# Optimization experiments

Hardware: AMD Instinct MI355X
Metric: run time of the kernel (lower is better)

## Reference

```python
import jax, jax.numpy as jnp
import numpy as np


def setup_inputs() -> dict:
    key = jax.random.key(0)
    k1, k2, k3, k4 = jax.random.split(key, 4)
    B, Q, K, H, D = 2, 2048, 2048, 16, 64
    qs = jax.random.normal(k1, (B, Q, H, D), dtype=jnp.float32)
    ks = jax.random.normal(k2, (B, K, H, D), dtype=jnp.float32)
    vs = jax.random.normal(k3, (B, K, H, D), dtype=jnp.float32)
    # valid lengths in [1, K] so no row is fully masked
    valid_lens = jnp.maximum(jax.random.randint(k4, (B,), 0, K + 1, dtype=jnp.int32), 1)
    return {"qs": qs, "ks": ks, "vs": vs, "valid_lens": valid_lens}


def reference(qs, ks, vs, valid_lens):
    # Faithful math of ScanAttention: scaled dot-product attention with a
    # per-batch key-validity mask (online-softmax scan == exact softmax).
    B, Q, H, D = qs.shape
    K = ks.shape[1]
    scale = 1.0 / jnp.sqrt(jnp.float32(D))
    # [B, H, Q, K]
    scores = jnp.einsum('bqhd,bkhd->bhqk', qs * scale, ks)
    ks_mask = jnp.arange(K)[None, :] < valid_lens[:, None]  # [B, K]
    scores = jnp.where(ks_mask[:, None, None, :], scores, -jnp.inf)
    attn = jax.nn.softmax(scores, axis=-1)
    out = jnp.einsum('bhqk,bkhd->bqhd', attn, vs)  # [B, Q, H, D]
    return out
```

## Files before the change

kernel.cpp:

```cpp
#include <hip/hip_runtime.h>
#include <hip/hip_bf16.h>

typedef __bf16 bf16t;
typedef bf16t bf16x4 __attribute__((ext_vector_type(4)));
typedef bf16t bf16x8 __attribute__((ext_vector_type(8)));
typedef float f32x2 __attribute__((ext_vector_type(2)));
typedef float f32x4 __attribute__((ext_vector_type(4)));
typedef float f32x16 __attribute__((ext_vector_type(16)));
typedef unsigned short u16x8 __attribute__((ext_vector_type(8)));
typedef unsigned int u32x4 __attribute__((ext_vector_type(4)));

#define NB 2
#define NQ 2048
#define NK 2048
#define NH 16
#define ND 64
#define HD (NH * ND)
#define KVBLK 64
#define NUNITS 512
#define SCALE_LOG2E 0.18033688011112042f
#define RESCALE_THR 8.0f

#define OPART_BYTES(n) ((size_t)(n) * 8388608ULL)
#define ML_BYTES(n)    ((size_t)(n) * 524288ULL)

__device__ inline unsigned cvt_pk_bf16(float a, float b) {
    unsigned r;
    asm("v_cvt_pk_bf16_f32 %0, %1, %2" : "=v"(r) : "v"(a), "v"(b));
    return r;
}

__device__ inline void plswap(unsigned& a, unsigned& b) {
#if __has_builtin(__builtin_amdgcn_permlane32_swap)
    auto r = __builtin_amdgcn_permlane32_swap(a, b, false, false);
    a = r[0]; b = r[1];
#else
    const unsigned as = __shfl_xor((int)a, 32);
    const unsigned bs = __shfl_xor((int)b, 32);
    const bool lh = (threadIdx.x & 32) != 0;
    const unsigned na = lh ? bs : a;
    const unsigned nb = lh ? b : as;
    a = na; b = nb;
#endif
}

template <int NSPLIT>
__global__ __launch_bounds__(256, 3)
void scan_attn(const float* __restrict__ qs, const float* __restrict__ ks,
               const float* __restrict__ vs, const int* __restrict__ vlen,
               float* __restrict__ out, char* __restrict__ ws)
{
    const int bid = blockIdx.x;
    const int x    = bid & 7;
    const int jj   = bid >> 3;
    const int b    = jj & 1;
    const int code = x | ((jj >> 1) << 3);
    const int qt   = code / (16 * NSPLIT);
    const int rr   = code % (16 * NSPLIT);
    const int h    = rr / NSPLIT;
    const int s    = rr % NSPLIT;
    const int uidx = ((b * NH + h) << 4) + qt;

    const int tid  = threadIdx.x;
    const int wq   = tid >> 6;
    const int lane = tid & 63;
    const int ql   = lane & 31;
    const int lh   = lane >> 5;
    const int swq  = (ql & 7) << 4;
    const int q    = qt * 128 + wq * 32 + ql;

    const int nkv    = vlen[b];
    const int ntiles = (nkv + KVBLK - 1) >> 6;
    const int rem    = nkv & 63;
    const int tlo    = (ntiles * s) / NSPLIT;
    const int thi    = (ntiles * (s + 1)) / NSPLIT;

    const float* qptr = qs + ((size_t)b * NQ + q) * HD + h * ND;
    const float* kptr = ks + (size_t)b * NK * HD + h * ND;
    const float* vptr = vs + (size_t)b * NK * HD + h * ND;

    __shared__ __align__(16) char smem[2][16384];

    bf16x8 qf[4];
#pragma unroll
    for (int c = 0; c < 4; ++c) {
        const float* p = qptr + 16 * c + 8 * lh;
        f32x4 lo4 = *reinterpret_cast<const f32x4*>(p);
        f32x4 hi4 = *reinterpret_cast<const f32x4*>(p + 4);
#pragma unroll
        for (int e = 0; e < 4; ++e) {
            qf[c][e]     = (bf16t)(lo4[e] * SCALE_LOG2E);
            qf[c][4 + e] = (bf16t)(hi4[e] * SCALE_LOG2E);
        }
    }

    const int skr  = tid >> 3;
    const int skc  = (tid & 7) << 3;
    const int skc2 = (tid & 7) << 4;
    const int ksw  = (skr & 7) << 4;
    const int svd  = tid & 63;
    const int svk8 = (tid >> 6) << 3;
    const int svk2 = (tid >> 6) << 4;
    const int vsw  = (svd & 7) << 4;

    f32x4 kreg[2];
    float vreg[8];

    auto load_half = [&](int kb, int half) {
        const float* kp = kptr + (size_t)(kb + half * 32 + skr) * HD + skc;
        kreg[0] = *reinterpret_cast<const f32x4*>(kp);
        kreg[1] = *reinterpret_cast<const f32x4*>(kp + 4);
        const float* vp = vptr + (size_t)(kb + half * 32 + svk8) * HD + svd;
#pragma unroll
        for (int e = 0; e < 8; ++e)
            vreg[e] = vp[(size_t)e * HD];
    };

    auto store_half = [&](int buf, int half) {
        u16x8 w0;
#pragma unroll
        for (int i = 0; i < 2; ++i)
#pragma unroll
            for (int e = 0; e < 4; ++e)
                w0[4 * i + e] = __builtin_bit_cast(unsigned short, (bf16t)kreg[i][e]);
        char* kb_ = smem[buf] + (half * 32 + skr) * 128;
        *reinterpret_cast<u16x8*>(kb_ + (skc2 ^ ksw)) = w0;

        u16x8 x0;
#pragma unroll
        for (int e = 0; e < 8; ++e)
            x0[e] = __builtin_bit_cast(unsigned short, (bf16t)vreg[e]);
        char* vb_ = smem[buf] + 8192 + svd * 128;
        *reinterpret_cast<u16x8*>(vb_ + ((svk2 + half * 64) ^ vsw)) = x0;
    };

    float mrun = -__builtin_inff();
    float lrun = 0.0f;
    f32x16 o[2] = {};

    if (tlo < thi) {
        load_half(tlo << 6, 0); store_half(0, 0);
        load_half(tlo << 6, 1); store_half(0, 1);
    }
    __syncthreads();

    int cur = 0;
    for (int t = tlo; t < thi; ++t) {
        const int kb = t << 6;
        const bool has_next = (t + 1) < thi;
        if (has_next) load_half((t + 1) << 6, 0);

        const char* kbuf = smem[cur];
        f32x16 s_[2];
#pragma unroll
        for (int h2 = 0; h2 < 2; ++h2) {
            f32x16 acc = {};
            const char* krow = kbuf + (32 * h2 + ql) * 128;
#pragma unroll
            for (int c = 0; c < 4; ++c) {
                bf16x8 kf = *reinterpret_cast<const bf16x8*>(
                    krow + ((32 * c + 16 * lh) ^ swq));
                acc = __builtin_amdgcn_mfma_f32_32x32x16_bf16(kf, qf[c], acc, 0, 0, 0);
            }
            s_[h2] = acc;
        }

        if (has_next) {
            store_half(cur ^ 1, 0);
            load_half((t + 1) << 6, 1);
        }

        if (rem && t == ntiles - 1) {
            const int krem = nkv - kb;
#pragma unroll
            for (int h2 = 0; h2 < 2; ++h2)
#pragma unroll
                for (int r = 0; r < 16; ++r)
                    if (32 * h2 + (r & 3) + 8 * (r >> 2) + 4 * lh >= krem)
                        s_[h2][r] = -__builtin_inff();
        }

        float pmax = -__builtin_inff();
#pragma unroll
        for (int h2 = 0; h2 < 2; ++h2)
#pragma unroll
            for (int r = 0; r < 16; ++r) pmax = fmaxf(pmax, s_[h2][r]);
        pmax = fmaxf(pmax, __shfl_xor(pmax, 32));

        if (!__all(pmax <= mrun + RESCALE_THR)) {
            const float mnew  = fmaxf(mrun, pmax);
            const float alpha = exp2f(mrun - mnew);
            lrun *= alpha;
            o[0] *= alpha;
            o[1] *= alpha;
            mrun = mnew;
        }

        float ps = 0.0f;
#pragma unroll
        for (int h2 = 0; h2 < 2; ++h2)
#pragma unroll
            for (int r = 0; r < 16; ++r) {
                const float pv = exp2f(s_[h2][r] - mrun);
                s_[h2][r] = pv;
                ps += pv;
            }
        ps += __shfl_xor(ps, 32);
        lrun += ps;

        bf16x8 pf[4];
#pragma unroll
        for (int c = 0; c < 4; ++c) {
            const int h2 = c >> 1, r0 = (c & 1) * 8;
            unsigned a0 = cvt_pk_bf16(s_[h2][r0 + 0], s_[h2][r0 + 1]);
            unsigned b0 = cvt_pk_bf16(s_[h2][r0 + 4], s_[h2][r0 + 5]);
            plswap(a0, b0);
            unsigned a1 = cvt_pk_bf16(s_[h2][r0 + 2], s_[h2][r0 + 3]);
            unsigned b1 = cvt_pk_bf16(s_[h2][r0 + 6], s_[h2][r0 + 7]);
            plswap(a1, b1);
            pf[c] = __builtin_bit_cast(bf16x8, (u32x4){a0, a1, b0, b1});
        }

        const char* vbuf = smem[cur] + 8192;
#pragma unroll
        for (int dt = 0; dt < 2; ++dt) {
            const char* vrow = vbuf + (32 * dt + ql) * 128;
#pragma unroll
            for (int c = 0; c < 4; ++c) {
                bf16x8 vf = *reinterpret_cast<const bf16x8*>(
                    vrow + ((32 * c + 16 * lh) ^ swq));
                o[dt] = __builtin_amdgcn_mfma_f32_32x32x16_bf16(vf, pf[c], o[dt], 0, 0, 0);
            }
        }

        if (has_next) store_half(cur ^ 1, 1);
        __syncthreads();
        cur ^= 1;
    }

    if (NSPLIT == 1) {
        const float inv = 1.0f / lrun;
        float* op = out + ((size_t)b * NQ + q) * HD + h * ND;
#pragma unroll
        for (int dt = 0; dt < 2; ++dt)
#pragma unroll
            for (int rg = 0; rg < 4; ++rg) {
                f32x4 w;
#pragma unroll
                for (int e = 0; e < 4; ++e) w[e] = o[dt][4 * rg + e] * inv;
                *reinterpret_cast<f32x4*>(op + 32 * dt + 8 * rg + 4 * lh) = w;
            }
    } else {
        const int p = uidx * NSPLIT + s;
        bf16t* op = (bf16t*)ws + ((size_t)p * 128 + wq * 32 + ql) * 64;
#pragma unroll
        for (int dt = 0; dt < 2; ++dt)
#pragma unroll
            for (int rg = 0; rg < 4; ++rg) {
                bf16x4 w;
#pragma unroll
                for (int e = 0; e < 4; ++e) w[e] = (bf16t)o[dt][4 * rg + e];
                *reinterpret_cast<bf16x4*>(op + 32 * dt + 8 * rg + 4 * lh) = w;
            }
        if (lh == 0) {
            f32x2* ml = (f32x2*)(ws + OPART_BYTES(NSPLIT));
            ml[p * 128 + wq * 32 + ql] = (f32x2){mrun, lrun};
        }
    }
}

template <int NSPLIT>
__global__ __launch_bounds__(256)
void merge_attn(const char* __restrict__ ws, float* __restrict__ out)
{
    const int u  = blockIdx.x;
    const int b  = u >> 8;
    const int h  = (u >> 4) & 15;
    const int qt = u & 15;
    const int tid = threadIdx.x;
    const int q  = tid >> 1;
    const int dh = (tid & 1) * 32;

    const bf16t* opart = (const bf16t*)ws;
    const f32x2* ml    = (const f32x2*)(ws + OPART_BYTES(NSPLIT));

    float m_s[NSPLIT], l_s[NSPLIT];
    float M = -__builtin_inff();
#pragma unroll
    for (int s = 0; s < NSPLIT; ++s) {
        f32x2 v = ml[(u * NSPLIT + s) * 128 + q];
        m_s[s] = v[0]; l_s[s] = v[1];
        M = fmaxf(M, v[0]);
    }
    float L = 0.0f, w_s[NSPLIT];
#pragma unroll
    for (int s = 0; s < NSPLIT; ++s) {
        w_s[s] = exp2f(m_s[s] - M);
        L += w_s[s] * l_s[s];
    }
    const float inv = 1.0f / L;

    float acc[32];
#pragma unroll
    for (int e = 0; e < 32; ++e) acc[e] = 0.0f;
#pragma unroll
    for (int s = 0; s < NSPLIT; ++s) {
        const bf16t* op = opart + ((size_t)(u * NSPLIT + s) * 128 + q) * 64 + dh;
#pragma unroll
        for (int c = 0; c < 4; ++c) {
            bf16x8 v8 = *reinterpret_cast<const bf16x8*>(op + 8 * c);
#pragma unroll
            for (int e = 0; e < 8; ++e)
                acc[8 * c + e] += w_s[s] * (float)v8[e];
        }
    }

    float* op = out + ((size_t)b * NQ + qt * 128 + q) * HD + h * ND + dh;
#pragma unroll
    for (int c = 0; c < 8; ++c) {
        f32x4 st;
#pragma unroll
        for (int e = 0; e < 4; ++e) st[e] = acc[4 * c + e] * inv;
        *reinterpret_cast<f32x4*>(op + 4 * c) = st;
    }
}

extern "C" void kernel_launch(void* const* d_in, const int* in_sizes, int n_in,
                              void* d_out, int out_size, void* d_ws, size_t ws_size,
                              hipStream_t stream)
{
    const float* qs   = (const float*)d_in[0];
    const float* ks   = (const float*)d_in[1];
    const float* vs   = (const float*)d_in[2];
    const int*   vlen = (const int*)d_in[3];
    float* out = (float*)d_out;
    char*  ws  = (char*)d_ws;

    const size_t need2 = OPART_BYTES(2) + ML_BYTES(2);

    if (ws_size >= need2) {
        scan_attn<2><<<NUNITS * 2, 256, 0, stream>>>(qs, ks, vs, vlen, out, ws);
        merge_attn<2><<<NUNITS, 256, 0, stream>>>(ws, out);
    } else {
        scan_attn<1><<<NUNITS, 256, 0, stream>>>(qs, ks, vs, vlen, out, ws);
    }
}
```

Measured before the change: 65.62 us.

## Process each 32-key half-tile through full softmax and PV before the next

Restructures the inner loop so each 32-key half of the KV tile goes through QK MFMA, masking, online-softmax update and PV MFMA before the next half starts. Only one f32x16 score accumulator is live at a time instead of two, which lowers register pressure. The launch bound changes from a min-blocks hint to amdgpu_waves_per_eu(3). The cost is doing the max, rescale check and cross-lane reductions twice per tile, and a finer-grained dependency chain between score and PV MFMAs.

```diff
diff --git a/kernel.cpp b/kernel.cpp
--- a/kernel.cpp
+++ b/kernel.cpp
@@ -45,7 +45,7 @@
 }
 
 template <int NSPLIT>
-__global__ __launch_bounds__(256, 3)
+__global__ __launch_bounds__(256) __attribute__((amdgpu_waves_per_eu(3)))
 void scan_attn(const float* __restrict__ qs, const float* __restrict__ ks,
                const float* __restrict__ vs, const int* __restrict__ vlen,
                float* __restrict__ out, char* __restrict__ ws)
@@ -151,85 +151,79 @@
         if (has_next) load_half((t + 1) << 6, 0);
 
         const char* kbuf = smem[cur];
-        f32x16 s_[2];
+        const char* vbuf = smem[cur] + 8192;
+
 #pragma unroll
         for (int h2 = 0; h2 < 2; ++h2) {
-            f32x16 acc = {};
+            f32x16 s_ = {};
             const char* krow = kbuf + (32 * h2 + ql) * 128;
 #pragma unroll
             for (int c = 0; c < 4; ++c) {
                 bf16x8 kf = *reinterpret_cast<const bf16x8*>(
                     krow + ((32 * c + 16 * lh) ^ swq));
-                acc = __builtin_amdgcn_mfma_f32_32x32x16_bf16(kf, qf[c], acc, 0, 0, 0);
-            }
-            s_[h2] = acc;
-        }
-
-        if (has_next) {
-            store_half(cur ^ 1, 0);
-            load_half((t + 1) << 6, 1);
-        }
-
-        if (rem && t == ntiles - 1) {
-            const int krem = nkv - kb;
-#pragma unroll
-            for (int h2 = 0; h2 < 2; ++h2)
+                s_ = __builtin_amdgcn_mfma_f32_32x32x16_bf16(kf, qf[c], s_, 0, 0, 0);
+            }
+
+            if (rem && t == ntiles - 1) {
+                const int krem = nkv - kb;
 #pragma unroll
                 for (int r = 0; r < 16; ++r)
                     if (32 * h2 + (r & 3) + 8 * (r >> 2) + 4 * lh >= krem)
-                        s_[h2][r] = -__builtin_inff();
-        }
-
-        float pmax = -__builtin_inff();
-#pragma unroll
-        for (int h2 = 0; h2 < 2; ++h2)
-#pragma unroll
-            for (int r = 0; r < 16; ++r) pmax = fmaxf(pmax, s_[h2][r]);
-        pmax = fmaxf(pmax, __shfl_xor(pmax, 32));
-
-        if (!__all(pmax <= mrun + RESCALE_THR)) {
-            const float mnew  = fmaxf(mrun, pmax);
-            const float alpha = exp2f(mrun - mnew);
-            lrun *= alpha;
-            o[0] *= alpha;
-            o[1] *= alpha;
-            mrun = mnew;
-        }
-
-        float ps = 0.0f;
-#pragma unroll
-        for (int h2 = 0; h2 < 2; ++h2)
+                        s_[r] = -__builtin_inff();
+            }
+
+            float pmax = -__builtin_inff();
+#pragma unroll
+            for (int r = 0; r < 16; ++r) pmax = fmaxf(pmax, s_[r]);
+            pmax = fmaxf(pmax, __shfl_xor(pmax, 32));
+
+            if (!__all(pmax <= mrun + RESCALE_THR)) {
+                const float mnew  = fmaxf(mrun, pmax);
+                const float alpha = exp2f(mrun - mnew);
+                lrun *= alpha;
+                o[0] *= alpha;
+                o[1] *= alpha;
+                mrun = mnew;
+            }
+
+            float ps = 0.0f;
 #pragma unroll
             for (int r = 0; r < 16; ++r) {
-                const float pv = exp2f(s_[h2][r] - mrun);
-                s_[h2][r] = pv;
+                const float pv = exp2f(s_[r] - mrun);
+                s_[r] = pv;
                 ps += pv;
             }
-        ps += __shfl_xor(ps, 32);
-        lrun += ps;
-
-        bf16x8 pf[4];
-#pragma unroll
-        for (int c = 0; c < 4; ++c) {
-            const int h2 = c >> 1, r0 = (c & 1) * 8;
-            unsigned a0 = cvt_pk_bf16(s_[h2][r0 + 0], s_[h2][r0 + 1]);
-            unsigned b0 = cvt_pk_bf16(s_[h2][r0 + 4], s_[h2][r0 + 5]);
-            plswap(a0, b0);
-            unsigned a1 = cvt_pk_bf16(s_[h2][r0 + 2], s_[h2][r0 + 3]);
-            unsigned b1 = cvt_pk_bf16(s_[h2][r0 + 6], s_[h2][r0 + 7]);
-            plswap(a1, b1);
-            pf[c] = __builtin_bit_cast(bf16x8, (u32x4){a0, a1, b0, b1});
-        }
-
-        const char* vbuf = smem[cur] + 8192;
-#pragma unroll
-        for (int dt = 0; dt < 2; ++dt) {
-            const char* vrow = vbuf + (32 * dt + ql) * 128;
-#pragma unroll
-            for (int c = 0; c < 4; ++c) {
-                bf16x8 vf = *reinterpret_cast<const bf16x8*>(
-                    vrow + ((32 * c + 16 * lh) ^ swq));
-                o[dt] = __builtin_amdgcn_mfma_f32_32x32x16_bf16(vf, pf[c], o[dt], 0, 0, 0);
+            ps += __shfl_xor(ps, 32);
+            lrun += ps;
+
+            bf16x8 pf[2];
+#pragma unroll
+            for (int cc = 0; cc < 2; ++cc) {
+                const int r0 = cc * 8;
+                unsigned a0 = cvt_pk_bf16(s_[r0 + 0], s_[r0 + 1]);
+                unsigned b0 = cvt_pk_bf16(s_[r0 + 4], s_[r0 + 5]);
+                plswap(a0, b0);
+                unsigned a1 = cvt_pk_bf16(s_[r0 + 2], s_[r0 + 3]);
+                unsigned b1 = cvt_pk_bf16(s_[r0 + 6], s_[r0 + 7]);
+                plswap(a1, b1);
+                pf[cc] = __builtin_bit_cast(bf16x8, (u32x4){a0, a1, b0, b1});
+            }
+
+#pragma unroll
+            for (int dt = 0; dt < 2; ++dt) {
+                const char* vrow = vbuf + (32 * dt + ql) * 128;
+#pragma unroll
+                for (int cc = 0; cc < 2; ++cc) {
+                    const int c = 2 * h2 + cc;
+                    bf16x8 vf = *reinterpret_cast<const bf16x8*>(
+                        vrow + ((32 * c + 16 * lh) ^ swq));
+                    o[dt] = __builtin_amdgcn_mfma_f32_32x32x16_bf16(vf, pf[cc], o[dt], 0, 0, 0);
+                }
+            }
+
+            if (h2 == 0 && has_next) {
+                store_half(cur ^ 1, 0);
+                load_half((t + 1) << 6, 1);
             }
         }
 
```

New measurement: 68.29 us. 1.04x slower.
